# Performance work log

Measured on AMD Instinct MI355X. Metric: run time of the kernel, lower is better.

The kernel has to match this reference:

```python
import jax, jax.numpy as jnp
import numpy as np
from jax.ops import segment_sum

N_NODES = 100000
N_EDGES = 1250000
F_IN = 64
F_OUT = 64


def setup_inputs() -> dict:
    key = jax.random.key(0)
    k1, k2, k3, k4, k5 = jax.random.split(key, 5)
    x = jax.random.normal(k1, (N_NODES, F_IN), dtype=jnp.float32)
    edge_index = jax.random.randint(k2, (2, N_EDGES), 0, N_NODES, dtype=jnp.int32)
    edge_weight = jax.random.uniform(k3, (2, N_EDGES, 1), dtype=jnp.float32)
    # glorot_uniform for Dense kernels [in, out]
    lim = float(np.sqrt(6.0 / (F_IN + F_OUT)))
    W_src = jax.random.uniform(k4, (F_IN, F_OUT), minval=-lim, maxval=lim, dtype=jnp.float32)
    W_dst = jax.random.uniform(k5, (F_IN, F_OUT), minval=-lim, maxval=lim, dtype=jnp.float32)
    b_src = jnp.zeros((F_OUT,), dtype=jnp.float32)
    b_dst = jnp.zeros((F_OUT,), dtype=jnp.float32)
    return {"x": x, "edge_index": edge_index, "edge_weight": edge_weight,
            "W_src": W_src, "W_dst": W_dst, "b_src": b_src, "b_dst": b_dst}


def reference(x, edge_index, edge_weight, W_src, W_dst, b_src, b_dst):
    num_nodes = x.shape[0]
    senders, receivers = edge_index[0], edge_index[1]
    ew_s2d, ew_d2s = edge_weight[0], edge_weight[1]  # [E, 1] each
    x_gather = x[senders]  # [E, F_IN]
    agg_s2d = segment_sum(x_gather * ew_s2d, receivers, num_segments=num_nodes)
    agg_d2s = segment_sum(x_gather * ew_d2s, receivers, num_segments=num_nodes)
    out_s2d = agg_s2d @ W_src + b_src
    out_d2s = agg_d2s @ W_dst + b_dst
    return (out_s2d, out_d2s)
```

## Files before the change

kernel.cpp:

```cpp
#include <hip/hip_runtime.h>
#include <hip/hip_fp16.h>

#define N_NODES 100000
#define N_EDGES 1250000
#define F 64
#define SCAN_CHUNK 1024
#define NBLK_SCAN ((N_NODES + SCAN_CHUNK - 1) / SCAN_CHUNK)
#define GPW 4
#define NPB 32
#define TP  33


__global__ __launch_bounds__(256) void hist_kernel(const int* __restrict__ ei,
                                                   int* __restrict__ counts,
                                                   int* __restrict__ rank) {
    int e = blockIdx.x * 256 + threadIdx.x;
    if (e < N_EDGES) rank[e] = atomicAdd(&counts[ei[N_EDGES + e]], 1);
}

__global__ __launch_bounds__(256) void scan_reduce_kernel(const int* __restrict__ counts,
                                                          int* __restrict__ partials) {
    int base = blockIdx.x * SCAN_CHUNK + threadIdx.x * 4;
    int s = 0;
    if (base + 3 < N_NODES) {
        int4 c = *(const int4*)&counts[base];
        s = c.x + c.y + c.z + c.w;
    }
    for (int d = 32; d > 0; d >>= 1) s += __shfl_down(s, d);
    __shared__ int lds[4];
    int lane = threadIdx.x & 63, wave = threadIdx.x >> 6;
    if (lane == 0) lds[wave] = s;
    __syncthreads();
    if (threadIdx.x == 0) partials[blockIdx.x] = lds[0] + lds[1] + lds[2] + lds[3];
}

__global__ __launch_bounds__(256) void scan_apply_kernel(const int* __restrict__ counts,
                                                         const int* __restrict__ partials,
                                                         int* __restrict__ off) {
    __shared__ int sh_red[4];
    __shared__ int sh_base;
    __shared__ int wsum[4];
    int t = threadIdx.x;
    int lane = t & 63, wave = t >> 6;

    int pp = 0;
    if (t < blockIdx.x && t < NBLK_SCAN) pp = partials[t];
    for (int d = 32; d > 0; d >>= 1) pp += __shfl_down(pp, d);
    if (lane == 0) sh_red[wave] = pp;
    __syncthreads();
    if (t == 0) sh_base = sh_red[0] + sh_red[1] + sh_red[2] + sh_red[3];

    int base = blockIdx.x * SCAN_CHUNK + t * 4;
    int4 c = {0, 0, 0, 0};
    bool act = (base + 3 < N_NODES);
    if (act) c = *(const int4*)&counts[base];
    int s = c.x + c.y + c.z + c.w;

    int xs = s;
    for (int d = 1; d < 64; d <<= 1) {
        int y = __shfl_up(xs, d);
        if (lane >= d) xs += y;
    }
    if (lane == 63) wsum[wave] = xs;
    __syncthreads();
    int pre = xs - s;
    for (int w = 0; w < wave; ++w) pre += wsum[w];
    pre += sh_base;

    if (act) {
        int o0 = pre, o1 = o0 + c.x, o2 = o1 + c.y, o3 = o2 + c.z;
        int4 o = {o0, o1, o2, o3};
        *(int4*)&off[base] = o;
        if (base + 4 == N_NODES) off[N_NODES] = o3 + c.w;
    }
}

__global__ __launch_bounds__(256) void permute_kernel(const int* __restrict__ ei,
                                                      const float* __restrict__ ew,
                                                      const int* __restrict__ off,
                                                      const int* __restrict__ rank,
                                                      int2* __restrict__ pay) {
    int e = blockIdx.x * 256 + threadIdx.x;
    if (e >= N_EDGES) return;
    int r = ei[N_EDGES + e];
    int pos = off[r] + rank[e];
    __half2 h = __floats2half2_rn(ew[e], ew[N_EDGES + e]);
    int2 p;
    p.x = ei[e];
    p.y = *(const int*)&h;
    pay[pos] = p;
}

__global__ __launch_bounds__(512, 4) void agg_gemm_kernel(
    const float* __restrict__ x, const int* __restrict__ off,
    const int2* __restrict__ pay,
    const float* __restrict__ Wsrc, const float* __restrict__ Wdst,
    const float* __restrict__ bsrc, const float* __restrict__ bdst,
    float* __restrict__ outA, float* __restrict__ outB)
{
    __shared__ float tA[F * TP];
    __shared__ float tB[F * TP];
    int t = threadIdx.x;
    int w = t >> 6;
    int lane = t & 63;
    int n0 = blockIdx.x * NPB + w * GPW;
    int nIB0 = w * GPW;

    int b[GPW + 1];
    #pragma unroll
    for (int j = 0; j <= GPW; ++j) b[j] = off[n0 + j];

    int i = b[0];
    const int end = b[GPW];
    int cur = 0;
    int next_b = b[1];
    float accA = 0.f, accB = 0.f;

#define FLUSH() { tA[lane * TP + nIB0 + cur] = accA;                  \
                  tB[lane * TP + nIB0 + cur] = accB;                  \
                  accA = 0.f; accB = 0.f; ++cur;                      \
                  next_b = (cur < GPW) ? b[cur + 1] : 0x7fffffff; }

    int2 pc[4]; float vc[4];
    if (i + 4 <= end) {
        #pragma unroll
        for (int j = 0; j < 4; ++j) pc[j] = pay[i + j];
        #pragma unroll
        for (int j = 0; j < 4; ++j) vc[j] = x[(size_t)pc[j].x * F + lane];
    }
    while (i + 8 <= end) {
        int2 pn[4]; float vn[4];
        #pragma unroll
        for (int j = 0; j < 4; ++j) pn[j] = pay[i + 4 + j];
        #pragma unroll
        for (int j = 0; j < 4; ++j) vn[j] = x[(size_t)pn[j].x * F + lane];
        #pragma unroll
        for (int j = 0; j < 4; ++j) {
            while (i + j == next_b) FLUSH();
            float2 wv = __half22float2(*(const __half2*)&pc[j].y);
            accA += vc[j] * wv.x; accB += vc[j] * wv.y;
        }
        i += 4;
        #pragma unroll
        for (int j = 0; j < 4; ++j) { pc[j] = pn[j]; vc[j] = vn[j]; }
    }
    if (i + 4 <= end) {
        #pragma unroll
        for (int j = 0; j < 4; ++j) {
            while (i + j == next_b) FLUSH();
            float2 wv = __half22float2(*(const __half2*)&pc[j].y);
            accA += vc[j] * wv.x; accB += vc[j] * wv.y;
        }
        i += 4;
    }
    while (i < end) {
        while (i == next_b) FLUSH();
        int2 p = pay[i];
        float2 wv = __half22float2(*(const __half2*)&p.y);
        float v = x[(size_t)p.x * F + lane];
        accA += v * wv.x; accB += v * wv.y;
        ++i;
    }
    while (cur < GPW) FLUSH();
#undef FLUSH

    __syncthreads();

    if (t < 256) {
        int dir = t >> 7;
        int tx = t & 15, ty = (t >> 4) & 7;
        int j4 = tx * 4, n4 = ty * 4;
        const float* W    = dir ? Wdst : Wsrc;
        const float* bias = dir ? bdst : bsrc;
        const float* tile = dir ? tB : tA;
        float* out        = dir ? outB : outA;

        float4 bj = *(const float4*)&bias[j4];
        float4 a0 = bj, a1 = bj, a2 = bj, a3 = bj;
        #pragma unroll 8
        for (int k = 0; k < F; ++k) {
            float4 wv = *(const float4*)&W[k * F + j4];
            float v0 = tile[k * TP + n4 + 0];
            float v1 = tile[k * TP + n4 + 1];
            float v2 = tile[k * TP + n4 + 2];
            float v3 = tile[k * TP + n4 + 3];
            a0.x += v0 * wv.x; a0.y += v0 * wv.y; a0.z += v0 * wv.z; a0.w += v0 * wv.w;
            a1.x += v1 * wv.x; a1.y += v1 * wv.y; a1.z += v1 * wv.z; a1.w += v1 * wv.w;
            a2.x += v2 * wv.x; a2.y += v2 * wv.y; a2.z += v2 * wv.z; a2.w += v2 * wv.w;
            a3.x += v3 * wv.x; a3.y += v3 * wv.y; a3.z += v3 * wv.z; a3.w += v3 * wv.w;
        }
        int nb = blockIdx.x * NPB + n4;
        *(float4*)&out[(size_t)(nb + 0) * F + j4] = a0;
        *(float4*)&out[(size_t)(nb + 1) * F + j4] = a1;
        *(float4*)&out[(size_t)(nb + 2) * F + j4] = a2;
        *(float4*)&out[(size_t)(nb + 3) * F + j4] = a3;
    }
}


__global__ __launch_bounds__(256) void scatter_fallback(const float4* __restrict__ x4,
                                                        const int* __restrict__ ei,
                                                        const float* __restrict__ ew,
                                                        float* __restrict__ aggA,
                                                        float* __restrict__ aggB) {
    int t = blockIdx.x * blockDim.x + threadIdx.x;
    int e = t >> 4;
    int lane16 = t & 15;
    if (e >= N_EDGES) return;
    int src = ei[e], dst = ei[N_EDGES + e];
    float w0 = ew[e], w1 = ew[N_EDGES + e];
    float4 v = x4[(size_t)src * 16 + lane16];
    int base = dst * F + lane16 * 4;
    atomicAdd(&aggA[base + 0], v.x * w0); atomicAdd(&aggA[base + 1], v.y * w0);
    atomicAdd(&aggA[base + 2], v.z * w0); atomicAdd(&aggA[base + 3], v.w * w0);
    atomicAdd(&aggB[base + 0], v.x * w1); atomicAdd(&aggB[base + 1], v.y * w1);
    atomicAdd(&aggB[base + 2], v.z * w1); atomicAdd(&aggB[base + 3], v.w * w1);
}

__global__ __launch_bounds__(256) void matmul_fallback(float* __restrict__ outA, float* __restrict__ outB,
                                                       const float* __restrict__ Wsrc, const float* __restrict__ Wdst,
                                                       const float* __restrict__ bsrc, const float* __restrict__ bdst) {
    __shared__ float lWs[F * F];
    __shared__ float lWd[F * F];
    for (int i = threadIdx.x; i < F * F / 4; i += blockDim.x) {
        ((float4*)lWs)[i] = ((const float4*)Wsrc)[i];
        ((float4*)lWd)[i] = ((const float4*)Wdst)[i];
    }
    __syncthreads();
    int wave = (blockIdx.x * blockDim.x + threadIdx.x) >> 6;
    int lane = threadIdx.x & 63;
    if (wave >= N_NODES) return;
    size_t rowbase = (size_t)wave * F;
    float a0 = outA[rowbase + lane], a1 = outB[rowbase + lane];
    float acc0 = bsrc[lane], acc1 = bdst[lane];
    #pragma unroll
    for (int k = 0; k < F; ++k) {
        acc0 += __shfl(a0, k) * lWs[k * F + lane];
        acc1 += __shfl(a1, k) * lWd[k * F + lane];
    }
    outA[rowbase + lane] = acc0;
    outB[rowbase + lane] = acc1;
}


extern "C" void kernel_launch(void* const* d_in, const int* in_sizes, int n_in,
                              void* d_out, int out_size, void* d_ws, size_t ws_size,
                              hipStream_t stream) {
    const float* x    = (const float*)d_in[0];
    const int*   ei   = (const int*)d_in[1];
    const float* ew   = (const float*)d_in[2];
    const float* Wsrc = (const float*)d_in[3];
    const float* Wdst = (const float*)d_in[4];
    const float* bsrc = (const float*)d_in[5];
    const float* bdst = (const float*)d_in[6];

    float* outA = (float*)d_out;
    float* outB = (float*)d_out + (size_t)N_NODES * F;

    const size_t OFF_COUNTS   = 0;
    const size_t OFF_OFF      = 400128;
    const size_t OFF_PARTIALS = 800640;
    const size_t OFF_RANK     = 801152;
    const size_t OFF_PAY      = 5801152;
    const size_t REQ          = 15801152;

    if (ws_size >= REQ) {
        char* ws = (char*)d_ws;
        int*  counts   = (int*)(ws + OFF_COUNTS);
        int*  off      = (int*)(ws + OFF_OFF);
        int*  partials = (int*)(ws + OFF_PARTIALS);
        int*  rank     = (int*)(ws + OFF_RANK);
        int2* pay      = (int2*)(ws + OFF_PAY);

        hipMemsetAsync(counts, 0, (size_t)N_NODES * sizeof(int), stream);

        int eblk = (N_EDGES + 255) / 256;
        hist_kernel<<<eblk, 256, 0, stream>>>(ei, counts, rank);
        scan_reduce_kernel<<<NBLK_SCAN, 256, 0, stream>>>(counts, partials);
        scan_apply_kernel<<<NBLK_SCAN, 256, 0, stream>>>(counts, partials, off);
        permute_kernel<<<eblk, 256, 0, stream>>>(ei, ew, off, rank, pay);
        agg_gemm_kernel<<<N_NODES / NPB, 512, 0, stream>>>(
            x, off, pay, Wsrc, Wdst, bsrc, bdst, outA, outB);
    } else {
        hipMemsetAsync(d_out, 0, (size_t)out_size * sizeof(float), stream);
        int blocks_scatter = (N_EDGES * 16 + 255) / 256;
        scatter_fallback<<<blocks_scatter, 256, 0, stream>>>((const float4*)x, ei, ew, outA, outB);
        int blocks_mm = (N_NODES * 64 + 255) / 256;
        matmul_fallback<<<blocks_mm, 256, 0, stream>>>(outA, outB, Wsrc, Wdst, bsrc, bdst);
    }
}
```

Measured before the change: 260.8 us.

## Assign one node per 16-lane quarter-wave with float4 gathers in aggregation

The aggregation kernel now gives each destination node to 16 lanes, each loading a float4 of the source row, instead of having a full 64-lane wave walk four nodes serially with scalar loads and boundary flush checks. A two-deep software prefetch overlaps the next gathers with the current accumulation. Blocks shrink to 256 threads covering 16 nodes, and the fused 64x64 GEMM epilogue is retiled to two nodes per thread. This removes the per-edge boundary branching and widens memory transactions, at the cost of load imbalance within a wave when degrees differ across the four nodes it holds.

```diff
diff --git a/kernel.cpp b/kernel.cpp
--- a/kernel.cpp
+++ b/kernel.cpp
@@ -6,9 +6,8 @@
 #define F 64
 #define SCAN_CHUNK 1024
 #define NBLK_SCAN ((N_NODES + SCAN_CHUNK - 1) / SCAN_CHUNK)
-#define GPW 4
-#define NPB 32
-#define TP  33
+#define NPB 16
+#define TP 18
 
 
 __global__ __launch_bounds__(256) void hist_kernel(const int* __restrict__ ei,
@@ -91,7 +90,7 @@
     pay[pos] = p;
 }
 
-__global__ __launch_bounds__(512, 4) void agg_gemm_kernel(
+__global__ __launch_bounds__(256, 8) void agg_gemm_kernel(
     const float* __restrict__ x, const int* __restrict__ off,
     const int2* __restrict__ pay,
     const float* __restrict__ Wsrc, const float* __restrict__ Wdst,
@@ -103,98 +102,68 @@
     int t = threadIdx.x;
     int w = t >> 6;
     int lane = t & 63;
-    int n0 = blockIdx.x * NPB + w * GPW;
-    int nIB0 = w * GPW;
-
-    int b[GPW + 1];
+    int g = lane >> 4;
+    int l4 = lane & 15;
+    int nIB = w * 4 + g;
+    int n = blockIdx.x * NPB + nIB;
+
+    const float4* x4 = (const float4*)x;
+    int beg = off[n];
+    int end = off[n + 1];
+
+    float4 accA = {0.f, 0.f, 0.f, 0.f};
+    float4 accB = {0.f, 0.f, 0.f, 0.f};
+
+    if (beg < end) {
+        int last = end - 1;
+        int2 p0 = pay[beg];
+        float4 x0 = x4[(size_t)p0.x * 16 + l4];
+        int i1 = min(beg + 1, last);
+        int2 p1 = pay[i1];
+        float4 x1 = x4[(size_t)p1.x * 16 + l4];
+        for (int i = beg; i < end; ++i) {
+            int i2 = min(i + 2, last);
+            int2 p2 = pay[i2];
+            float4 x2 = x4[(size_t)p2.x * 16 + l4];
+            float2 wv = __half22float2(*(const __half2*)&p0.y);
+            accA.x += x0.x * wv.x; accA.y += x0.y * wv.x;
+            accA.z += x0.z * wv.x; accA.w += x0.w * wv.x;
+            accB.x += x0.x * wv.y; accB.y += x0.y * wv.y;
+            accB.z += x0.z * wv.y; accB.w += x0.w * wv.y;
+            p0 = p1; x0 = x1;
+            p1 = p2; x1 = x2;
+        }
+    }
+
     #pragma unroll
-    for (int j = 0; j <= GPW; ++j) b[j] = off[n0 + j];
-
-    int i = b[0];
-    const int end = b[GPW];
-    int cur = 0;
-    int next_b = b[1];
-    float accA = 0.f, accB = 0.f;
-
-#define FLUSH() { tA[lane * TP + nIB0 + cur] = accA;                  \
-                  tB[lane * TP + nIB0 + cur] = accB;                  \
-                  accA = 0.f; accB = 0.f; ++cur;                      \
-                  next_b = (cur < GPW) ? b[cur + 1] : 0x7fffffff; }
-
-    int2 pc[4]; float vc[4];
-    if (i + 4 <= end) {
-        #pragma unroll
-        for (int j = 0; j < 4; ++j) pc[j] = pay[i + j];
-        #pragma unroll
-        for (int j = 0; j < 4; ++j) vc[j] = x[(size_t)pc[j].x * F + lane];
-    }
-    while (i + 8 <= end) {
-        int2 pn[4]; float vn[4];
-        #pragma unroll
-        for (int j = 0; j < 4; ++j) pn[j] = pay[i + 4 + j];
-        #pragma unroll
-        for (int j = 0; j < 4; ++j) vn[j] = x[(size_t)pn[j].x * F + lane];
-        #pragma unroll
-        for (int j = 0; j < 4; ++j) {
-            while (i + j == next_b) FLUSH();
-            float2 wv = __half22float2(*(const __half2*)&pc[j].y);
-            accA += vc[j] * wv.x; accB += vc[j] * wv.y;
-        }
-        i += 4;
-        #pragma unroll
-        for (int j = 0; j < 4; ++j) { pc[j] = pn[j]; vc[j] = vn[j]; }
-    }
-    if (i + 4 <= end) {
-        #pragma unroll
-        for (int j = 0; j < 4; ++j) {
-            while (i + j == next_b) FLUSH();
-            float2 wv = __half22float2(*(const __half2*)&pc[j].y);
-            accA += vc[j] * wv.x; accB += vc[j] * wv.y;
-        }
-        i += 4;
-    }
-    while (i < end) {
-        while (i == next_b) FLUSH();
-        int2 p = pay[i];
-        float2 wv = __half22float2(*(const __half2*)&p.y);
-        float v = x[(size_t)p.x * F + lane];
-        accA += v * wv.x; accB += v * wv.y;
-        ++i;
-    }
-    while (cur < GPW) FLUSH();
-#undef FLUSH
-
-    __syncthreads();
-
-    if (t < 256) {
-        int dir = t >> 7;
-        int tx = t & 15, ty = (t >> 4) & 7;
-        int j4 = tx * 4, n4 = ty * 4;
-        const float* W    = dir ? Wdst : Wsrc;
-        const float* bias = dir ? bdst : bsrc;
-        const float* tile = dir ? tB : tA;
-        float* out        = dir ? outB : outA;
-
-        float4 bj = *(const float4*)&bias[j4];
-        float4 a0 = bj, a1 = bj, a2 = bj, a3 = bj;
-        #pragma unroll 8
-        for (int k = 0; k < F; ++k) {
-            float4 wv = *(const float4*)&W[k * F + j4];
-            float v0 = tile[k * TP + n4 + 0];
-            float v1 = tile[k * TP + n4 + 1];
-            float v2 = tile[k * TP + n4 + 2];
-            float v3 = tile[k * TP + n4 + 3];
-            a0.x += v0 * wv.x; a0.y += v0 * wv.y; a0.z += v0 * wv.z; a0.w += v0 * wv.w;
-            a1.x += v1 * wv.x; a1.y += v1 * wv.y; a1.z += v1 * wv.z; a1.w += v1 * wv.w;
-            a2.x += v2 * wv.x; a2.y += v2 * wv.y; a2.z += v2 * wv.z; a2.w += v2 * wv.w;
-            a3.x += v3 * wv.x; a3.y += v3 * wv.y; a3.z += v3 * wv.z; a3.w += v3 * wv.w;
-        }
-        int nb = blockIdx.x * NPB + n4;
-        *(float4*)&out[(size_t)(nb + 0) * F + j4] = a0;
-        *(float4*)&out[(size_t)(nb + 1) * F + j4] = a1;
-        *(float4*)&out[(size_t)(nb + 2) * F + j4] = a2;
-        *(float4*)&out[(size_t)(nb + 3) * F + j4] = a3;
-    }
+    for (int c = 0; c < 4; ++c) {
+        tA[(4 * l4 + c) * TP + nIB] = ((const float*)&accA)[c];
+        tB[(4 * l4 + c) * TP + nIB] = ((const float*)&accB)[c];
+    }
+
+    __syncthreads();
+
+    int dir = t >> 7;
+    int tx = t & 15;
+    int ty = (t >> 4) & 7;
+    const float* W    = dir ? Wdst : Wsrc;
+    const float* bias = dir ? bdst : bsrc;
+    const float* tile = dir ? tB : tA;
+    float* out        = dir ? outB : outA;
+    int j4 = tx * 4, n2 = ty * 2;
+
+    float4 bj = *(const float4*)&bias[j4];
+    float4 a0 = bj, a1 = bj;
+    #pragma unroll 8
+    for (int k = 0; k < F; ++k) {
+        float4 wv = *(const float4*)&W[k * F + j4];
+        float2 v  = *(const float2*)&tile[k * TP + n2];
+        a0.x += v.x * wv.x; a0.y += v.x * wv.y; a0.z += v.x * wv.z; a0.w += v.x * wv.w;
+        a1.x += v.y * wv.x; a1.y += v.y * wv.y; a1.z += v.y * wv.z; a1.w += v.y * wv.w;
+    }
+    int nb = blockIdx.x * NPB + n2;
+    *(float4*)&out[(size_t)(nb + 0) * F + j4] = a0;
+    *(float4*)&out[(size_t)(nb + 1) * F + j4] = a1;
 }
 
 
@@ -279,7 +248,7 @@
         scan_reduce_kernel<<<NBLK_SCAN, 256, 0, stream>>>(counts, partials);
         scan_apply_kernel<<<NBLK_SCAN, 256, 0, stream>>>(counts, partials, off);
         permute_kernel<<<eblk, 256, 0, stream>>>(ei, ew, off, rank, pay);
-        agg_gemm_kernel<<<N_NODES / NPB, 512, 0, stream>>>(
+        agg_gemm_kernel<<<N_NODES / NPB, 256, 0, stream>>>(
             x, off, pay, Wsrc, Wdst, bsrc, bdst, outA, outB);
     } else {
         hipMemsetAsync(d_out, 0, (size_t)out_size * sizeof(float), stream);
```

Result: no change. 255.9 us (-1.9%).
